# Optimization experiments

Measured on AMD Instinct MI355X. Metric: run time of the kernel, lower is better.

## Reference

```python
import jax, jax.numpy as jnp
import numpy as np

NEG_SLOPE = 0.2

def setup_inputs() -> dict:
    key = jax.random.key(0)
    k1, k2, k3, k4 = jax.random.split(key, 4)
    bs, n, f_in, f_out, n_head = 8, 2048, 64, 32, 4
    h = jax.random.normal(k1, (bs, n, f_in), dtype=jnp.float32)
    # xavier_uniform-like scales (exact init values irrelevant for correctness baseline)
    w = jax.random.normal(k2, (n_head, f_in, f_out), dtype=jnp.float32) * 0.14
    a_src = jax.random.normal(k3, (n_head, f_out, 1), dtype=jnp.float32) * 0.3
    a_dst = jax.random.normal(k4, (n_head, f_out, 1), dtype=jnp.float32) * 0.3
    b = jnp.zeros((f_out,), dtype=jnp.float32)
    return {"h": h, "w": w, "a_src": a_src, "a_dst": a_dst, "b": b}

def reference(h, w, a_src, a_dst, b):
    # h: [bs, n, f_in]; w: [H, f_in, f_out]
    h_prime = jnp.einsum('bnf,hfo->bhno', h, w)            # [bs, H, n, f_out]
    attn_src = jnp.einsum('bhno,hot->bhnt', h_prime, a_src)  # [bs, H, n, 1]
    attn_dst = jnp.einsum('bhno,hot->bhnt', h_prime, a_dst)  # [bs, H, n, 1]
    # additive broadcast: score[b,h,i,j] = src[i] + dst[j]
    attn = attn_src + jnp.swapaxes(attn_dst, -1, -2)        # [bs, H, n, n]
    attn = jnp.where(attn >= 0, attn, NEG_SLOPE * attn)     # leaky relu
    attn = jax.nn.softmax(attn, axis=-1)
    # dropout p=0.0 -> identity
    output = jnp.einsum('bhnm,bhmo->bhno', attn, h_prime) + b
    return (output, attn)
```

## Files before the change

kernel.cpp:

```cpp
#include <hip/hip_runtime.h>
#include <hip/hip_bf16.h>

typedef __bf16 bf16x8 __attribute__((ext_vector_type(8)));
typedef float  f32x4  __attribute__((ext_vector_type(4)));

#define LOG2E 1.4426950408889634f

__device__ __forceinline__ float lrelu(float x) { return x >= 0.f ? x : 0.2f * x; }

__device__ __forceinline__ float exp2f_fast(float x) {
#if __has_builtin(__builtin_amdgcn_exp2f)
    return __builtin_amdgcn_exp2f(x);
#else
    return __expf(x * 0.6931471805599453f);
#endif
}

__device__ __forceinline__ unsigned short bfbits(float x) {
    __hip_bfloat16 h = __float2bfloat16(x);
    return *reinterpret_cast<unsigned short*>(&h);
}

__device__ __forceinline__ unsigned packE(float d) {
    const unsigned b1 = bfbits(exp2f_fast(d));
    const unsigned b2 = bfbits(exp2f_fast(0.2f * d));
    return (b1 << 16) | b2;
}

__global__ __launch_bounds__(256) void k_hprime(
    const float* __restrict__ hg,
    const float* __restrict__ wg,
    const float* __restrict__ a_src,
    const float* __restrict__ a_dst,
    __hip_bfloat16* __restrict__ hpF,
    float* __restrict__ srcv,
    float* __restrict__ dstv)
{
    __shared__ float w_lds[64 * 32];
    __shared__ float h_lds[64 * 64];
    __shared__ __hip_bfloat16 t_lds[32 * 72];

    const int t  = threadIdx.x;
    const int bh = blockIdx.x >> 5;
    const int n0 = (blockIdx.x & 31) * 64;
    const int b  = bh >> 2, hh = bh & 3;

    {
        const float4* s4 = (const float4*)(wg + hh * 2048);
        float4* d4 = (float4*)w_lds;
        d4[t] = s4[t];
        d4[t + 256] = s4[t + 256];
        const float4* s4h = (const float4*)(hg + ((size_t)(b * 2048 + n0)) * 64);
        float4* d4h = (float4*)h_lds;
#pragma unroll
        for (int k = 0; k < 4; k++) d4h[t + 256 * k] = s4h[t + 256 * k];
    }
    __syncthreads();

    const int o  = t & 31;
    const int nb = t >> 5;
    float acc[8];
#pragma unroll
    for (int k = 0; k < 8; k++) acc[k] = 0.f;
    for (int f = 0; f < 64; f++) {
        const float wv = w_lds[f * 32 + o];
#pragma unroll
        for (int k = 0; k < 8; k++)
            acc[k] = fmaf(h_lds[(nb + 8 * k) * 64 + f], wv, acc[k]);
    }
    const float as = a_src[hh * 32 + o] * LOG2E;
    const float ad = a_dst[hh * 32 + o] * LOG2E;
#pragma unroll
    for (int k = 0; k < 8; k++) {
        float sv = acc[k] * as;
        float dv = acc[k] * ad;
#pragma unroll
        for (int m = 16; m >= 1; m >>= 1) {
            sv += __shfl_xor(sv, m);
            dv += __shfl_xor(dv, m);
        }
        if (o == 0) {
            const int n = n0 + nb + 8 * k;
            srcv[bh * 2048 + n] = sv;
            dstv[bh * 2048 + n] = dv;
        }
    }
#pragma unroll
    for (int k = 0; k < 8; k++)
        t_lds[o * 72 + nb + 8 * k] = __float2bfloat16(acc[k]);
    __syncthreads();
    {
        const int oo = t >> 3;
        const int ch = t & 7;
        const int jb = ch >> 2, g = ch & 3;
        const __hip_bfloat16* src0 = &t_lds[oo * 72 + jb * 32 + g * 4];
        union { unsigned long long q[2]; uint4 v; } u;
        u.q[0] = *(const unsigned long long*)(src0);
        u.q[1] = *(const unsigned long long*)(src0 + 16);
        *(uint4*)(hpF + ((size_t)(bh * 32 + oo)) * 2048 + n0 + ch * 8) = u.v;
    }
}

__global__ __launch_bounds__(256) void k_main(
    const __hip_bfloat16* __restrict__ hpF,
    const float* __restrict__ srcv,
    const float* __restrict__ dstv,
    const float* __restrict__ bias,
    float* __restrict__ outp,
    float* __restrict__ attn)
{
    __shared__ __attribute__((aligned(16))) float    d_lds[2048];
    __shared__ __attribute__((aligned(16))) unsigned e12[2048];
    __shared__ float ns_lds[64], a1_lds[64], a2_lds[64];
    __shared__ float red[4];

    const int t    = threadIdx.x;
    const int role = blockIdx.x & 1;
    const int wid  = blockIdx.x >> 1;
    const int bh   = wid >> 5;
    const int row0 = (wid & 31) * 64;

    float lmax = -1e30f;
    {
        const float4* s4 = (const float4*)(dstv + bh * 2048);
        float4* d4 = (float4*)d_lds;
#pragma unroll
        for (int k = 0; k < 2; k++) {
            const float4 v = s4[t + 256 * k];
            d4[t + 256 * k] = v;
            lmax = fmaxf(lmax, fmaxf(fmaxf(v.x, v.y), fmaxf(v.z, v.w)));
        }
    }
#pragma unroll
    for (int m = 32; m >= 1; m >>= 1) lmax = fmaxf(lmax, __shfl_xor(lmax, m));
    if ((t & 63) == 0) red[t >> 6] = lmax;
    __syncthreads();
    const float dmax = fmaxf(fmaxf(red[0], red[1]), fmaxf(red[2], red[3]));

    {
#pragma unroll
        for (int k = 0; k < 2; k++) {
            const float4 dv = *((const float4*)d_lds + t + 256 * k);
            uint4 u;
            u.x = packE(dv.x); u.y = packE(dv.y);
            u.z = packE(dv.z); u.w = packE(dv.w);
            *((uint4*)e12 + t + 256 * k) = u;
        }
    }
    __syncthreads();

    {
        const int r = t >> 2, q = t & 3;
        const float s  = srcv[bh * 2048 + row0 + r];
        const float ns = -s;
        float acc1 = 0.f, acc2 = 0.f;
        for (int it = 0; it < 128; it++) {
            const int j = q * 4 + it * 16;
            const float4 dv = *(const float4*)(d_lds + j);
            const uint4  uv = *(const uint4*)(e12 + j);
            { const bool c = dv.x >= ns; acc1 += c ? __uint_as_float(uv.x & 0xffff0000u) : 0.f; acc2 += c ? 0.f : __uint_as_float(uv.x << 16); }
            { const bool c = dv.y >= ns; acc1 += c ? __uint_as_float(uv.y & 0xffff0000u) : 0.f; acc2 += c ? 0.f : __uint_as_float(uv.y << 16); }
            { const bool c = dv.z >= ns; acc1 += c ? __uint_as_float(uv.z & 0xffff0000u) : 0.f; acc2 += c ? 0.f : __uint_as_float(uv.z << 16); }
            { const bool c = dv.w >= ns; acc1 += c ? __uint_as_float(uv.w & 0xffff0000u) : 0.f; acc2 += c ? 0.f : __uint_as_float(uv.w << 16); }
        }
        acc1 += __shfl_xor(acc1, 1); acc1 += __shfl_xor(acc1, 2);
        acc2 += __shfl_xor(acc2, 1); acc2 += __shfl_xor(acc2, 2);
        if (q == 0) {
            const float m  = lrelu(s + dmax);
            const float f1 = exp2f_fast(s - m);
            const float f2 = exp2f_fast(0.2f * s - m);
            const float is = 1.f / (f1 * acc1 + f2 * acc2);
            ns_lds[r] = ns; a1_lds[r] = f1 * is; a2_lds[r] = f2 * is;
        }
    }
    __syncthreads();

    if (role == 0) {
        float* rowbase = attn + ((size_t)(bh * 2048) + row0) * 2048;
        for (int r = 0; r < 64; r++) {
            const float ns = ns_lds[r], a1 = a1_lds[r], a2 = a2_lds[r];
            float* rp = rowbase + (size_t)r * 2048;
#pragma unroll
            for (int h2 = 0; h2 < 2; h2++) {
                const int j = t * 4 + h2 * 1024;
                const float4 dv = *(const float4*)(d_lds + j);
                const uint4  uv = *(const uint4*)(e12 + j);
                f32x4 p;
                { const bool c = dv.x >= ns; p[0] = (c ? a1 : a2) * __uint_as_float(c ? (uv.x & 0xffff0000u) : (uv.x << 16)); }
                { const bool c = dv.y >= ns; p[1] = (c ? a1 : a2) * __uint_as_float(c ? (uv.y & 0xffff0000u) : (uv.y << 16)); }
                { const bool c = dv.z >= ns; p[2] = (c ? a1 : a2) * __uint_as_float(c ? (uv.z & 0xffff0000u) : (uv.z << 16)); }
                { const bool c = dv.w >= ns; p[3] = (c ? a1 : a2) * __uint_as_float(c ? (uv.w & 0xffff0000u) : (uv.w << 16)); }
                __builtin_nontemporal_store(p, (f32x4*)(rp + j));
            }
        }
    } else {
        const int l  = t & 63, w = t >> 6;
        const int lr = l & 15, g = l >> 4;
        const int rA = w * 16 + lr;
        const float ns = ns_lds[rA], a1 = a1_lds[rA], a2 = a2_lds[rA];
        const __hip_bfloat16* hb0 = hpF + ((size_t)(bh * 32 + lr)) * 2048;
        const __hip_bfloat16* hb1 = hpF + ((size_t)(bh * 32 + 16 + lr)) * 2048;
        f32x4 acc0 = {0.f, 0.f, 0.f, 0.f};
        f32x4 acc1v = {0.f, 0.f, 0.f, 0.f};
        for (int jb = 0; jb < 64; jb++) {
            const int j = jb * 32 + g * 4;
            const float4 dA = *(const float4*)(d_lds + j);
            const float4 dB = *(const float4*)(d_lds + j + 16);
            const uint4  uA = *(const uint4*)(e12 + j);
            const uint4  uB = *(const uint4*)(e12 + j + 16);
            union { unsigned short us[8]; bf16x8 v; } A;
            { const bool c = dA.x >= ns; A.us[0] = bfbits((c ? a1 : a2) * __uint_as_float(c ? (uA.x & 0xffff0000u) : (uA.x << 16))); }
            { const bool c = dA.y >= ns; A.us[1] = bfbits((c ? a1 : a2) * __uint_as_float(c ? (uA.y & 0xffff0000u) : (uA.y << 16))); }
            { const bool c = dA.z >= ns; A.us[2] = bfbits((c ? a1 : a2) * __uint_as_float(c ? (uA.z & 0xffff0000u) : (uA.z << 16))); }
            { const bool c = dA.w >= ns; A.us[3] = bfbits((c ? a1 : a2) * __uint_as_float(c ? (uA.w & 0xffff0000u) : (uA.w << 16))); }
            { const bool c = dB.x >= ns; A.us[4] = bfbits((c ? a1 : a2) * __uint_as_float(c ? (uB.x & 0xffff0000u) : (uB.x << 16))); }
            { const bool c = dB.y >= ns; A.us[5] = bfbits((c ? a1 : a2) * __uint_as_float(c ? (uB.y & 0xffff0000u) : (uB.y << 16))); }
            { const bool c = dB.z >= ns; A.us[6] = bfbits((c ? a1 : a2) * __uint_as_float(c ? (uB.z & 0xffff0000u) : (uB.z << 16))); }
            { const bool c = dB.w >= ns; A.us[7] = bfbits((c ? a1 : a2) * __uint_as_float(c ? (uB.w & 0xffff0000u) : (uB.w << 16))); }
            const bf16x8 b0 = *(const bf16x8*)(hb0 + jb * 32 + g * 8);
            const bf16x8 b1 = *(const bf16x8*)(hb1 + jb * 32 + g * 8);
            acc0  = __builtin_amdgcn_mfma_f32_16x16x32_bf16(A.v, b0, acc0, 0, 0, 0);
            acc1v = __builtin_amdgcn_mfma_f32_16x16x32_bf16(A.v, b1, acc1v, 0, 0, 0);
        }
        const float b0v = bias[lr];
        const float b1v = bias[16 + lr];
#pragma unroll
        for (int reg = 0; reg < 4; reg++) {
            const int grow = row0 + w * 16 + g * 4 + reg;
            float* op = outp + ((size_t)(bh * 2048) + grow) * 32;
            op[lr]      = acc0[reg] + b0v;
            op[16 + lr] = acc1v[reg] + b1v;
        }
    }
}

extern "C" void kernel_launch(void* const* d_in, const int* in_sizes, int n_in,
                              void* d_out, int out_size, void* d_ws, size_t ws_size,
                              hipStream_t stream) {
    (void)in_sizes; (void)n_in; (void)out_size; (void)ws_size;
    const float* h     = (const float*)d_in[0];
    const float* w     = (const float*)d_in[1];
    const float* a_src = (const float*)d_in[2];
    const float* a_dst = (const float*)d_in[3];
    const float* b     = (const float*)d_in[4];

    float* out  = (float*)d_out;
    float* attn = out + (size_t)8 * 4 * 2048 * 32;

    __hip_bfloat16* hpF = (__hip_bfloat16*)d_ws;
    float* srcv = (float*)((char*)d_ws + (size_t)32 * 32 * 2048 * 2);
    float* dstv = srcv + 32 * 2048;

    k_hprime<<<1024, 256, 0, stream>>>(h, w, a_src, a_dst, hpF, srcv, dstv);
    k_main  <<<2048, 256, 0, stream>>>(hpF, srcv, dstv, b, out, attn);
}
```

Measured before the change: 147.8 us.

## Split fused attention kernel into separate PV and attention-write kernels

The combined kernel, where paired blocks each recomputed row softmax stats and then either wrote the attention matrix or did the PV MFMA, is split in two. The first kernel computes the stats once per 64-row block, stores them to workspace and does the PV product. A second kernel of 256 blocks, each covering 256 rows, reads the stats and streams the dense attention matrix to memory. This removes the duplicated stat computation and gives the store-bound write phase its own launch shape, at the cost of an extra launch and a small workspace round trip.

```diff
diff --git a/kernel.cpp b/kernel.cpp
--- a/kernel.cpp
+++ b/kernel.cpp
@@ -101,13 +101,13 @@
     }
 }
 
-__global__ __launch_bounds__(256) void k_main(
+__global__ __launch_bounds__(256) void k_pv(
     const __hip_bfloat16* __restrict__ hpF,
     const float* __restrict__ srcv,
     const float* __restrict__ dstv,
     const float* __restrict__ bias,
     float* __restrict__ outp,
-    float* __restrict__ attn)
+    float* __restrict__ ws_ns, float* __restrict__ ws_a1, float* __restrict__ ws_a2)
 {
     __shared__ __attribute__((aligned(16))) float    d_lds[2048];
     __shared__ __attribute__((aligned(16))) unsigned e12[2048];
@@ -115,8 +115,7 @@
     __shared__ float red[4];
 
     const int t    = threadIdx.x;
-    const int role = blockIdx.x & 1;
-    const int wid  = blockIdx.x >> 1;
+    const int wid  = blockIdx.x;
     const int bh   = wid >> 5;
     const int row0 = (wid & 31) * 64;
 
@@ -170,30 +169,15 @@
             const float f1 = exp2f_fast(s - m);
             const float f2 = exp2f_fast(0.2f * s - m);
             const float is = 1.f / (f1 * acc1 + f2 * acc2);
-            ns_lds[r] = ns; a1_lds[r] = f1 * is; a2_lds[r] = f2 * is;
-        }
-    }
-    __syncthreads();
-
-    if (role == 0) {
-        float* rowbase = attn + ((size_t)(bh * 2048) + row0) * 2048;
-        for (int r = 0; r < 64; r++) {
-            const float ns = ns_lds[r], a1 = a1_lds[r], a2 = a2_lds[r];
-            float* rp = rowbase + (size_t)r * 2048;
-#pragma unroll
-            for (int h2 = 0; h2 < 2; h2++) {
-                const int j = t * 4 + h2 * 1024;
-                const float4 dv = *(const float4*)(d_lds + j);
-                const uint4  uv = *(const uint4*)(e12 + j);
-                f32x4 p;
-                { const bool c = dv.x >= ns; p[0] = (c ? a1 : a2) * __uint_as_float(c ? (uv.x & 0xffff0000u) : (uv.x << 16)); }
-                { const bool c = dv.y >= ns; p[1] = (c ? a1 : a2) * __uint_as_float(c ? (uv.y & 0xffff0000u) : (uv.y << 16)); }
-                { const bool c = dv.z >= ns; p[2] = (c ? a1 : a2) * __uint_as_float(c ? (uv.z & 0xffff0000u) : (uv.z << 16)); }
-                { const bool c = dv.w >= ns; p[3] = (c ? a1 : a2) * __uint_as_float(c ? (uv.w & 0xffff0000u) : (uv.w << 16)); }
-                __builtin_nontemporal_store(p, (f32x4*)(rp + j));
-            }
-        }
-    } else {
+            const float a1 = f1 * is, a2 = f2 * is;
+            ns_lds[r] = ns; a1_lds[r] = a1; a2_lds[r] = a2;
+            const int gr = bh * 2048 + row0 + r;
+            ws_ns[gr] = ns; ws_a1[gr] = a1; ws_a2[gr] = a2;
+        }
+    }
+    __syncthreads();
+
+    {
         const int l  = t & 63, w = t >> 6;
         const int lr = l & 15, g = l >> 4;
         const int rA = w * 16 + lr;
@@ -234,6 +218,56 @@
     }
 }
 
+__global__ __launch_bounds__(256) void k_write(
+    const float* __restrict__ dstv,
+    const float* __restrict__ ws_ns, const float* __restrict__ ws_a1, const float* __restrict__ ws_a2,
+    float* __restrict__ attn)
+{
+    __shared__ __attribute__((aligned(16))) float    d_lds[2048];
+    __shared__ __attribute__((aligned(16))) unsigned e12[2048];
+    __shared__ float cns[256], ca1[256], ca2[256];
+
+    const int t  = threadIdx.x;
+    const int bh = blockIdx.x >> 3;
+    const int r0 = (blockIdx.x & 7) * 256;
+
+    {
+        const float4* s4 = (const float4*)(dstv + bh * 2048);
+#pragma unroll
+        for (int k = 0; k < 2; k++) {
+            const float4 v = s4[t + 256 * k];
+            *((float4*)d_lds + t + 256 * k) = v;
+            uint4 u;
+            u.x = packE(v.x); u.y = packE(v.y);
+            u.z = packE(v.z); u.w = packE(v.w);
+            *((uint4*)e12 + t + 256 * k) = u;
+        }
+        const int gr = bh * 2048 + r0 + t;
+        cns[t] = ws_ns[gr]; ca1[t] = ws_a1[gr]; ca2[t] = ws_a2[gr];
+    }
+    __syncthreads();
+
+    const int w = t >> 6, l = t & 63;
+    float* base = attn + ((size_t)(bh * 2048) + r0 + w * 64) * 2048;
+    for (int rr = 0; rr < 64; rr++) {
+        const int lrow = w * 64 + rr;
+        const float ns = cns[lrow], a1 = ca1[lrow], a2 = ca2[lrow];
+        float* rp = base + (size_t)rr * 2048;
+#pragma unroll
+        for (int seg = 0; seg < 8; seg++) {
+            const int j = seg * 256 + l * 4;
+            const float4 dv = *(const float4*)(d_lds + j);
+            const uint4  uv = *(const uint4*)(e12 + j);
+            f32x4 p;
+            { const bool c = dv.x >= ns; p[0] = (c ? a1 : a2) * __uint_as_float(c ? (uv.x & 0xffff0000u) : (uv.x << 16)); }
+            { const bool c = dv.y >= ns; p[1] = (c ? a1 : a2) * __uint_as_float(c ? (uv.y & 0xffff0000u) : (uv.y << 16)); }
+            { const bool c = dv.z >= ns; p[2] = (c ? a1 : a2) * __uint_as_float(c ? (uv.z & 0xffff0000u) : (uv.z << 16)); }
+            { const bool c = dv.w >= ns; p[3] = (c ? a1 : a2) * __uint_as_float(c ? (uv.w & 0xffff0000u) : (uv.w << 16)); }
+            __builtin_nontemporal_store(p, (f32x4*)(rp + j));
+        }
+    }
+}
+
 extern "C" void kernel_launch(void* const* d_in, const int* in_sizes, int n_in,
                               void* d_out, int out_size, void* d_ws, size_t ws_size,
                               hipStream_t stream) {
@@ -247,10 +281,15 @@
     float* out  = (float*)d_out;
     float* attn = out + (size_t)8 * 4 * 2048 * 32;
 
-    __hip_bfloat16* hpF = (__hip_bfloat16*)d_ws;
-    float* srcv = (float*)((char*)d_ws + (size_t)32 * 32 * 2048 * 2);
-    float* dstv = srcv + 32 * 2048;
+    char* wsb = (char*)d_ws;
+    __hip_bfloat16* hpF = (__hip_bfloat16*)wsb;
+    float* srcv  = (float*)(wsb + (4u << 20));
+    float* dstv  = srcv + 32 * 2048;
+    float* ws_ns = dstv + 32 * 2048;
+    float* ws_a1 = ws_ns + 32 * 2048;
+    float* ws_a2 = ws_a1 + 32 * 2048;
 
     k_hprime<<<1024, 256, 0, stream>>>(h, w, a_src, a_dst, hpF, srcv, dstv);
-    k_main  <<<2048, 256, 0, stream>>>(hpF, srcv, dstv, b, out, attn);
-}
+    k_pv    <<<1024, 256, 0, stream>>>(hpF, srcv, dstv, b, out, ws_ns, ws_a1, ws_a2);
+    k_write <<< 256, 256, 0, stream>>>(dstv, ws_ns, ws_a1, ws_a2, attn);
+}
```

After: 201.7 us. 1.36x slower.
